# Kernel optimization log

Measured on AMD Instinct MI355X. Metric: run time of the kernel, lower is better.

## Reference

```python
import jax, jax.numpy as jnp
import numpy as np

H = 16
D_HEAD = 64  # model_dim // head_count = 1024 // 16
MODEL_DIM = 1024
MODEL_DIM1 = 768


def setup_inputs() -> dict:
    key = jax.random.key(0)
    ks = jax.random.split(key, 12)
    B, Q, K = 4, 1024, 1024
    inp = {
        "key": jax.random.normal(ks[0], (B, K, MODEL_DIM), jnp.float32),
        "value": jax.random.normal(ks[1], (B, K, MODEL_DIM), jnp.float32),
        "query": jax.random.normal(ks[2], (B, Q, MODEL_DIM1), jnp.float32),
        "mask": jax.random.randint(ks[3], (B, Q), 0, 2, jnp.int32),
        "additional_mask": jax.random.randint(ks[4], (B, K), 0, 2, jnp.int32),
        # learned params (nn.Linear weights stored as [in, out] for x @ W)
        "Wk": 0.02 * jax.random.normal(ks[5], (MODEL_DIM, H * D_HEAD), jnp.float32),
        "bk": jnp.zeros((H * D_HEAD,), jnp.float32),
        "Wv": 0.02 * jax.random.normal(ks[6], (MODEL_DIM, H * D_HEAD), jnp.float32),
        "bv": jnp.zeros((H * D_HEAD,), jnp.float32),
        "Wq": 0.02 * jax.random.normal(ks[7], (MODEL_DIM1, H * D_HEAD), jnp.float32),
        "bq": jnp.zeros((H * D_HEAD,), jnp.float32),
        "Wo": 0.02 * jax.random.normal(ks[8], (H * D_HEAD, MODEL_DIM1), jnp.float32),
        "bo": jnp.zeros((MODEL_DIM1,), jnp.float32),
    }
    return inp


def reference(key, value, query, mask, additional_mask, Wk, bk, Wv, bv, Wq, bq, Wo, bo):
    B, K_len = key.shape[0], key.shape[1]
    Q_len = query.shape[1]

    def shape(x):  # [B, L, H*d] -> [B, H, L, d]
        return x.reshape(B, -1, H, D_HEAD).transpose(0, 2, 1, 3)

    k = shape(key @ Wk + bk)
    v = shape(value @ Wv + bv)
    q = shape(query @ Wq + bq) / jnp.sqrt(jnp.float32(D_HEAD))

    scores = jnp.einsum("bhqd,bhkd->bhqk", q, k)  # [B,H,Q,K]
    top_score = scores[:, 0, :, :]  # pre-mask scores of head 0

    neg = jnp.float32(-1e18)
    scores = jnp.where(mask[:, None, :, None] == 0, neg, scores)
    scores = jnp.where(additional_mask[:, None, None, :] == 0, neg, scores)

    attn = jax.nn.softmax(scores, axis=-1)
    # dropout omitted (eval mode / deterministic reference)
    ctx = jnp.einsum("bhqk,bhkd->bhqd", attn, v)
    ctx = ctx.transpose(0, 2, 1, 3).reshape(B, Q_len, H * D_HEAD)
    output = ctx @ Wo + bo
    return output, top_score
```

## Files before the change

kernel.cpp:

```cpp
#include <hip/hip_runtime.h>
#include <hip/hip_bf16.h>

typedef __bf16 bf16_t;
typedef __bf16 bf16x8 __attribute__((ext_vector_type(8)));
typedef __bf16 bf16x4 __attribute__((ext_vector_type(4)));
typedef __bf16 bf16x2 __attribute__((ext_vector_type(2)));
typedef float  f32x4  __attribute__((ext_vector_type(4)));

#define MFMA16(a,b,c) __builtin_amdgcn_mfma_f32_16x16x32_bf16((a),(b),(c),0,0,0)

static constexpr int Bn = 4, Hn = 16, Dh = 64, SEQ = 1024;

template<int KD, int N, int MODE, typename AT>
__global__ __launch_bounds__(256)
void gemm_kernel(const AT* __restrict__ A, const float* __restrict__ W,
                 const float* __restrict__ bias, void* __restrict__ outp,
                 float scale)
{
    constexpr int BM = 128, BN = 64, BK = 32;
    __shared__ bf16_t As[BM][40];
    __shared__ bf16_t Bs[BN][40];
    const int t = threadIdx.x;
    const int lane = t & 63;
    const int w = t >> 6;
    const int wr = w >> 1, wc = w & 1;
    const int row0 = blockIdx.y * BM;
    const int col0 = blockIdx.x * BN;
    const int lrow = lane & 15;
    const int lk8  = (lane >> 4) * 8;

    const int ar = t >> 1, ac = (t & 1) * 16;
    const int bn0 = (t & 15) * 4, bk0 = (t >> 4) * 2;

    f32x4 acc[4][2] = {};

    f32x4  a_f[4];
    bf16x8 a_h[2];
    f32x4  b_r[2];

    auto loadA = [&](int kk) {
        if constexpr (sizeof(AT) == 4) {
            const float* src = (const float*)A + (size_t)(row0 + ar) * KD + kk + ac;
            a_f[0] = *(const f32x4*)(src + 0);
            a_f[1] = *(const f32x4*)(src + 4);
            a_f[2] = *(const f32x4*)(src + 8);
            a_f[3] = *(const f32x4*)(src + 12);
        } else {
            const bf16_t* src = (const bf16_t*)A + (size_t)(row0 + ar) * KD + kk + ac;
            a_h[0] = *(const bf16x8*)(src);
            a_h[1] = *(const bf16x8*)(src + 8);
        }
    };
    auto loadB = [&](int kk) {
        const float* src = W + (size_t)(kk + bk0) * N + col0 + bn0;
        b_r[0] = *(const f32x4*)(src);
        b_r[1] = *(const f32x4*)(src + N);
    };
    auto storeA = [&]() {
        bf16x8 v0, v1;
        if constexpr (sizeof(AT) == 4) {
            #pragma unroll
            for (int j = 0; j < 4; j++) {
                v0[j]     = (bf16_t)a_f[0][j];
                v0[4 + j] = (bf16_t)a_f[1][j];
                v1[j]     = (bf16_t)a_f[2][j];
                v1[4 + j] = (bf16_t)a_f[3][j];
            }
        } else { v0 = a_h[0]; v1 = a_h[1]; }
        *(bf16x8*)&As[ar][ac]     = v0;
        *(bf16x8*)&As[ar][ac + 8] = v1;
    };
    auto storeB = [&]() {
        #pragma unroll
        for (int c = 0; c < 4; c++) {
            bf16x2 p;
            p[0] = (bf16_t)b_r[0][c];
            p[1] = (bf16_t)b_r[1][c];
            *(bf16x2*)&Bs[bn0 + c][bk0] = p;
        }
    };

    loadA(0); loadB(0);
    for (int kk = 0; kk < KD; kk += BK) {
        storeA(); storeB();
        __syncthreads();
        if (kk + BK < KD) { loadA(kk + BK); loadB(kk + BK); }
        bf16x8 af[4], bfr[2];
        #pragma unroll
        for (int mf = 0; mf < 4; mf++)
            af[mf] = *(const bf16x8*)&As[wr * 64 + mf * 16 + lrow][lk8];
        #pragma unroll
        for (int nf = 0; nf < 2; nf++)
            bfr[nf] = *(const bf16x8*)&Bs[wc * 32 + nf * 16 + lrow][lk8];
        #pragma unroll
        for (int mf = 0; mf < 4; mf++)
            #pragma unroll
            for (int nf = 0; nf < 2; nf++)
                acc[mf][nf] = MFMA16(af[mf], bfr[nf], acc[mf][nf]);
        __syncthreads();
    }

    #pragma unroll
    for (int mf = 0; mf < 4; mf++) {
        #pragma unroll
        for (int nf = 0; nf < 2; nf++) {
            const int gcol = col0 + wc * 32 + nf * 16 + lrow;
            const float bv = bias[gcol];
            #pragma unroll
            for (int r = 0; r < 4; r++) {
                const int grow = row0 + wr * 64 + mf * 16 + (lane >> 4) * 4 + r;
                const float v = (acc[mf][nf][r] + bv) * scale;
                if constexpr (MODE == 0) {
                    const int b = grow >> 10, s = grow & 1023;
                    const int h = gcol >> 6, d = gcol & 63;
                    ((bf16_t*)outp)[((size_t)(b * Hn + h) * SEQ + s) * Dh + d] = (bf16_t)v;
                } else if constexpr (MODE == 1) {
                    const int b = grow >> 10, s = grow & 1023;
                    const int h = gcol >> 6, d = gcol & 63;
                    ((bf16_t*)outp)[((size_t)(b * Hn + h) * Dh + d) * SEQ + s] = (bf16_t)v;
                } else {
                    ((float*)outp)[(size_t)grow * N + gcol] = v;
                }
            }
        }
    }
}

__global__ __launch_bounds__(256)
void attn_kernel(const bf16_t* __restrict__ kbuf, const bf16_t* __restrict__ vT,
                 const bf16_t* __restrict__ qbuf, const int* __restrict__ qmask,
                 const int* __restrict__ kmask, bf16_t* __restrict__ ctx,
                 float* __restrict__ topsc)
{
    __shared__ bf16_t Pall[4][16 * 64];
    const int t = threadIdx.x, lane = t & 63, w = t >> 6;
    const int bidx = blockIdx.x;
    const int qt = bidx & 15, bh = bidx >> 4, b = bh >> 4, h = bh & 15;
    const int lrow = lane & 15, lk4 = lane >> 4, lk8 = lk4 * 8;
    const int wrow0 = qt * 64 + w * 16;
    const bf16_t* kb = kbuf + (size_t)bh * SEQ * Dh;
    const bf16_t* vb = vT + (size_t)bh * Dh * SEQ;
    char* Pw = (char*)&Pall[w][0];

    bf16x8 aq0, aq1;
    {
        const bf16_t* qp = qbuf + ((size_t)bh * SEQ + wrow0 + lrow) * Dh + lk8;
        aq0 = *(const bf16x8*)(qp);
        aq1 = *(const bf16x8*)(qp + 32);
    }
    int qmk[4];
    #pragma unroll
    for (int r = 0; r < 4; r++) qmk[r] = qmask[b * SEQ + wrow0 + lk4 * 4 + r];

    float m_run[4], l_run[4];
    #pragma unroll
    for (int r = 0; r < 4; r++) { m_run[r] = -__builtin_inff(); l_run[r] = 0.f; }
    f32x4 o[4] = {};

    bf16x8 kc0[4], kc1[4];
    #pragma unroll
    for (int nf = 0; nf < 4; nf++) {
        const bf16_t* kp = kb + (size_t)(nf * 16 + lrow) * Dh + lk8;
        kc0[nf] = *(const bf16x8*)(kp);
        kc1[nf] = *(const bf16x8*)(kp + 32);
    }

    for (int kt = 0; kt < 16; kt++) {
        const int key0 = kt * 64;
        bf16x8 vf0[4], vf1[4];
        #pragma unroll
        for (int nf = 0; nf < 4; nf++) {
            const bf16_t* vp = vb + (size_t)(nf * 16 + lrow) * SEQ + key0 + lk8;
            vf0[nf] = *(const bf16x8*)(vp);
            vf1[nf] = *(const bf16x8*)(vp + 32);
        }
        f32x4 s[4] = {};
        #pragma unroll
        for (int nf = 0; nf < 4; nf++) {
            s[nf] = MFMA16(aq0, kc0[nf], s[nf]);
            s[nf] = MFMA16(aq1, kc1[nf], s[nf]);
        }
        bf16x8 kn0[4], kn1[4];
        if (kt < 15) {
            #pragma unroll
            for (int nf = 0; nf < 4; nf++) {
                const bf16_t* kp = kb + (size_t)(key0 + 64 + nf * 16 + lrow) * Dh + lk8;
                kn0[nf] = *(const bf16x8*)(kp);
                kn1[nf] = *(const bf16x8*)(kp + 32);
            }
        }
        if (h == 0) {
            #pragma unroll
            for (int nf = 0; nf < 4; nf++)
                #pragma unroll
                for (int r = 0; r < 4; r++)
                    topsc[((size_t)b * SEQ + wrow0 + lk4 * 4 + r) * SEQ +
                          key0 + nf * 16 + lrow] = s[nf][r];
        }
        int km[4];
        #pragma unroll
        for (int nf = 0; nf < 4; nf++)
            km[nf] = kmask[b * SEQ + key0 + nf * 16 + lrow];
        float p[4][4], mt[4];
        #pragma unroll
        for (int r = 0; r < 4; r++) mt[r] = -__builtin_inff();
        #pragma unroll
        for (int nf = 0; nf < 4; nf++)
            #pragma unroll
            for (int r = 0; r < 4; r++) {
                const float sv = (qmk[r] && km[nf]) ? s[nf][r] : -1e18f;
                p[nf][r] = sv;
                mt[r] = fmaxf(mt[r], sv);
            }
        #pragma unroll
        for (int d = 1; d < 16; d <<= 1)
            #pragma unroll
            for (int r = 0; r < 4; r++) mt[r] = fmaxf(mt[r], __shfl_xor(mt[r], d));
        float resc[4], rs[4];
        #pragma unroll
        for (int r = 0; r < 4; r++) {
            const float mn = fmaxf(m_run[r], mt[r]);
            resc[r] = __expf(m_run[r] - mn);
            m_run[r] = mn;
            rs[r] = 0.f;
        }
        #pragma unroll
        for (int nf = 0; nf < 4; nf++)
            #pragma unroll
            for (int r = 0; r < 4; r++) {
                p[nf][r] = __expf(p[nf][r] - m_run[r]);
                rs[r] += p[nf][r];
            }
        #pragma unroll
        for (int d = 1; d < 16; d <<= 1)
            #pragma unroll
            for (int r = 0; r < 4; r++) rs[r] += __shfl_xor(rs[r], d);
        #pragma unroll
        for (int r = 0; r < 4; r++) l_run[r] = l_run[r] * resc[r] + rs[r];
        #pragma unroll
        for (int nf = 0; nf < 4; nf++)
            #pragma unroll
            for (int r = 0; r < 4; r++) o[nf][r] *= resc[r];
        #pragma unroll
        for (int nf = 0; nf < 4; nf++)
            #pragma unroll
            for (int r = 0; r < 4; r++) {
                const int prow = lk4 * 4 + r;
                const int pcol = nf * 16 + lrow;
                *(bf16_t*)(Pw + prow * 128 + ((pcol * 2) ^ ((prow & 7) << 4))) =
                    (bf16_t)p[nf][r];
            }
        bf16x8 pa[2];
        #pragma unroll
        for (int ks = 0; ks < 2; ks++) {
            const int coff = (ks * 32 + lk8) * 2;
            pa[ks] = *(const bf16x8*)(Pw + lrow * 128 + (coff ^ ((lrow & 7) << 4)));
        }
        #pragma unroll
        for (int nf = 0; nf < 4; nf++) {
            o[nf] = MFMA16(pa[0], vf0[nf], o[nf]);
            o[nf] = MFMA16(pa[1], vf1[nf], o[nf]);
        }
        #pragma unroll
        for (int nf = 0; nf < 4; nf++) { kc0[nf] = kn0[nf]; kc1[nf] = kn1[nf]; }
    }
    #pragma unroll
    for (int nf = 0; nf < 4; nf++)
        #pragma unroll
        for (int r = 0; r < 4; r++) {
            const int grow = wrow0 + lk4 * 4 + r;
            const float val = o[nf][r] / l_run[r];
            ctx[((size_t)b * SEQ + grow) * (Hn * Dh) + h * Dh + nf * 16 + lrow] =
                (bf16_t)val;
        }
}

extern "C" void kernel_launch(void* const* d_in, const int* in_sizes, int n_in,
                              void* d_out, int out_size, void* d_ws, size_t ws_size,
                              hipStream_t stream)
{
    const float* key   = (const float*)d_in[0];
    const float* value = (const float*)d_in[1];
    const float* query = (const float*)d_in[2];
    const int*   mask  = (const int*)d_in[3];
    const int*   amask = (const int*)d_in[4];
    const float* Wk = (const float*)d_in[5];
    const float* bk = (const float*)d_in[6];
    const float* Wv = (const float*)d_in[7];
    const float* bv = (const float*)d_in[8];
    const float* Wq = (const float*)d_in[9];
    const float* bq = (const float*)d_in[10];
    const float* Wo = (const float*)d_in[11];
    const float* bo = (const float*)d_in[12];

    const size_t per = (size_t)Bn * Hn * SEQ * Dh;
    bf16_t* kbuf = (bf16_t*)d_ws;
    bf16_t* vT   = kbuf + per;
    bf16_t* qbuf = vT + per;
    bf16_t* ctx  = qbuf + per;

    float* outf  = (float*)d_out;
    float* topsc = outf + (size_t)Bn * SEQ * 768;

    gemm_kernel<1024, 1024, 0, float><<<dim3(16, 32), 256, 0, stream>>>(key, Wk, bk, kbuf, 1.0f);
    gemm_kernel<1024, 1024, 1, float><<<dim3(16, 32), 256, 0, stream>>>(value, Wv, bv, vT, 1.0f);
    gemm_kernel<768, 1024, 0, float><<<dim3(16, 32), 256, 0, stream>>>(query, Wq, bq, qbuf, 0.125f);
    attn_kernel<<<dim3(Bn * Hn * 16), 256, 0, stream>>>(kbuf, vT, qbuf, mask, amask, ctx, topsc);
    gemm_kernel<1024, 768, 2, bf16_t><<<dim3(12, 32), 256, 0, stream>>>(ctx, Wo, bo, outf, 1.0f);
}
```

Measured before the change: 350.0 us.

## Pre-transpose weights to bf16, double-buffer GEMMs, split top-score kernel

Adds a kernel that converts and transposes all four weight matrices to bf16 once per call, so the GEMM can stage B tiles with direct global-to-LDS loads into double-buffered shared memory. GEMM outputs for the Q/K/V projections go through an LDS tile so the head-split and transposed layouts are written with coalesced vector stores. The attention kernel swaps the MFMA operand order so each lane owns one query row, which removes most shuffle reductions and vectorises the mask and P stores. The head-0 score writes move out of attention into a separate kernel that recomputes Q·K. The transposed weights are parked in the top_score region of the output buffer and overwritten by the final kernel; the extra launches and the recomputation add cost.

```diff
diff --git a/kernel.cpp b/kernel.cpp
--- a/kernel.cpp
+++ b/kernel.cpp
@@ -4,122 +4,181 @@
 typedef __bf16 bf16_t;
 typedef __bf16 bf16x8 __attribute__((ext_vector_type(8)));
 typedef __bf16 bf16x4 __attribute__((ext_vector_type(4)));
-typedef __bf16 bf16x2 __attribute__((ext_vector_type(2)));
 typedef float  f32x4  __attribute__((ext_vector_type(4)));
+typedef int    i32x4  __attribute__((ext_vector_type(4)));
 
 #define MFMA16(a,b,c) __builtin_amdgcn_mfma_f32_16x16x32_bf16((a),(b),(c),0,0,0)
 
 static constexpr int Bn = 4, Hn = 16, Dh = 64, SEQ = 1024;
+
+__device__ __forceinline__ void gll16(const void* g, void* l) {
+    __builtin_amdgcn_global_load_lds(
+        (const __attribute__((address_space(1))) void*)g,
+        (__attribute__((address_space(3))) void*)l, 16, 0, 0);
+}
+
+__global__ __launch_bounds__(256)
+void wtrans_kernel(const float* __restrict__ s0, const float* __restrict__ s1,
+                   const float* __restrict__ s2, const float* __restrict__ s3,
+                   bf16_t* __restrict__ d0, bf16_t* __restrict__ d1,
+                   bf16_t* __restrict__ d2, bf16_t* __restrict__ d3)
+{
+    __shared__ bf16_t tile[64][72];
+    const int bid = blockIdx.x, t = threadIdx.x;
+    const float* src; bf16_t* dst; int R, C, tr, tc;
+    if (bid < 256)      { src = s0; dst = d0; R = 1024; C = 1024; tr = bid >> 4;        tc = bid & 15; }
+    else if (bid < 512) { src = s1; dst = d1; R = 1024; C = 1024; tr = (bid-256) >> 4;  tc = (bid-256) & 15; }
+    else if (bid < 704) { src = s2; dst = d2; R = 768;  C = 1024; tr = (bid-512) >> 4;  tc = (bid-512) & 15; }
+    else                { src = s3; dst = d3; R = 1024; C = 768;  tr = (bid-704) / 12;  tc = (bid-704) % 12; }
+    const int r0 = tr * 64, c0 = tc * 64;
+    const int lr = t >> 2, lc0 = (t & 3) * 16;
+    #pragma unroll
+    for (int i = 0; i < 4; i++) {
+        f32x4 v = *(const f32x4*)&src[(size_t)(r0 + lr) * C + c0 + lc0 + i * 4];
+        #pragma unroll
+        for (int j = 0; j < 4; j++) tile[lr][lc0 + i * 4 + j] = (bf16_t)v[j];
+    }
+    __syncthreads();
+    const int oc = t >> 2, orc0 = (t & 3) * 16;
+    #pragma unroll
+    for (int i = 0; i < 2; i++) {
+        bf16x8 vv;
+        #pragma unroll
+        for (int j = 0; j < 8; j++) vv[j] = tile[orc0 + i * 8 + j][oc];
+        *(bf16x8*)&dst[(size_t)(c0 + oc) * R + r0 + orc0 + i * 8] = vv;
+    }
+}
 
 template<int KD, int N, int MODE, typename AT>
 __global__ __launch_bounds__(256)
-void gemm_kernel(const AT* __restrict__ A, const float* __restrict__ W,
-                 const float* __restrict__ bias, void* __restrict__ outp,
-                 float scale)
-{
-    constexpr int BM = 128, BN = 64, BK = 32;
-    __shared__ bf16_t As[BM][40];
-    __shared__ bf16_t Bs[BN][40];
-    const int t = threadIdx.x;
-    const int lane = t & 63;
-    const int w = t >> 6;
+void gemm_bt(const AT* __restrict__ A, const bf16_t* __restrict__ Bt,
+             const float* __restrict__ bias, void* __restrict__ outp,
+             float scale)
+{
+    __shared__ bf16_t As[2][128 * 32];
+    __shared__ bf16_t Bs[2][64 * 32];
+    __shared__ bf16_t Ct[(MODE == 2) ? 1 : 128 * 72];
+    const int t = threadIdx.x, lane = t & 63, w = t >> 6;
     const int wr = w >> 1, wc = w & 1;
-    const int row0 = blockIdx.y * BM;
-    const int col0 = blockIdx.x * BN;
-    const int lrow = lane & 15;
-    const int lk8  = (lane >> 4) * 8;
-
+    const int row0 = blockIdx.y * 128, col0 = blockIdx.x * 64;
+    const int lrow = lane & 15, lk4 = lane >> 4, lk8 = lk4 * 8;
     const int ar = t >> 1, ac = (t & 1) * 16;
-    const int bn0 = (t & 15) * 4, bk0 = (t >> 4) * 2;
 
     f32x4 acc[4][2] = {};
-
-    f32x4  a_f[4];
-    bf16x8 a_h[2];
-    f32x4  b_r[2];
-
-    auto loadA = [&](int kk) {
+    f32x4 a_f[4];
+
+    auto aload = [&](int kk) {
         if constexpr (sizeof(AT) == 4) {
             const float* src = (const float*)A + (size_t)(row0 + ar) * KD + kk + ac;
-            a_f[0] = *(const f32x4*)(src + 0);
+            a_f[0] = *(const f32x4*)(src);
             a_f[1] = *(const f32x4*)(src + 4);
             a_f[2] = *(const f32x4*)(src + 8);
             a_f[3] = *(const f32x4*)(src + 12);
-        } else {
-            const bf16_t* src = (const bf16_t*)A + (size_t)(row0 + ar) * KD + kk + ac;
-            a_h[0] = *(const bf16x8*)(src);
-            a_h[1] = *(const bf16x8*)(src + 8);
         }
     };
-    auto loadB = [&](int kk) {
-        const float* src = W + (size_t)(kk + bk0) * N + col0 + bn0;
-        b_r[0] = *(const f32x4*)(src);
-        b_r[1] = *(const f32x4*)(src + N);
+    auto awrite = [&](int buf) {
+        if constexpr (sizeof(AT) == 4) {
+            bf16x8 v0, v1;
+            #pragma unroll
+            for (int j = 0; j < 4; j++) {
+                v0[j] = (bf16_t)a_f[0][j]; v0[4 + j] = (bf16_t)a_f[1][j];
+                v1[j] = (bf16_t)a_f[2][j]; v1[4 + j] = (bf16_t)a_f[3][j];
+            }
+            *(bf16x8*)&As[buf][ar * 32 + ac]     = v0;
+            *(bf16x8*)&As[buf][ar * 32 + ac + 8] = v1;
+        }
     };
-    auto storeA = [&]() {
-        bf16x8 v0, v1;
-        if constexpr (sizeof(AT) == 4) {
-            #pragma unroll
-            for (int j = 0; j < 4; j++) {
-                v0[j]     = (bf16_t)a_f[0][j];
-                v0[4 + j] = (bf16_t)a_f[1][j];
-                v1[j]     = (bf16_t)a_f[2][j];
-                v1[4 + j] = (bf16_t)a_f[3][j];
-            }
-        } else { v0 = a_h[0]; v1 = a_h[1]; }
-        *(bf16x8*)&As[ar][ac]     = v0;
-        *(bf16x8*)&As[ar][ac + 8] = v1;
+    auto astage_gll = [&](int buf, int kk) {
+        if constexpr (sizeof(AT) == 2) {
+            #pragma unroll
+            for (int j = 0; j < 2; j++) {
+                const int idx = j * 256 + t;
+                const bf16_t* g = (const bf16_t*)A +
+                    (size_t)(row0 + (idx >> 2)) * KD + kk + (idx & 3) * 8;
+                gll16(g, &As[buf][(j * 256 + w * 64) * 8]);
+            }
+        }
     };
-    auto storeB = [&]() {
-        #pragma unroll
-        for (int c = 0; c < 4; c++) {
-            bf16x2 p;
-            p[0] = (bf16_t)b_r[0][c];
-            p[1] = (bf16_t)b_r[1][c];
-            *(bf16x2*)&Bs[bn0 + c][bk0] = p;
-        }
+    auto bstage = [&](int buf, int kk) {
+        const bf16_t* g = Bt + (size_t)(col0 + (t >> 2)) * KD + kk + (t & 3) * 8;
+        gll16(g, &Bs[buf][w * 512]);
     };
 
-    loadA(0); loadB(0);
-    for (int kk = 0; kk < KD; kk += BK) {
-        storeA(); storeB();
+    constexpr int NB = KD / 32;
+    if constexpr (sizeof(AT) == 4) { aload(0); awrite(0); }
+    else                            astage_gll(0, 0);
+    bstage(0, 0);
+
+    for (int s = 0; s < NB; s++) {
         __syncthreads();
-        if (kk + BK < KD) { loadA(kk + BK); loadB(kk + BK); }
+        const int cur = s & 1;
+        if (s + 1 < NB) {
+            bstage(cur ^ 1, (s + 1) * 32);
+            if constexpr (sizeof(AT) == 4) aload((s + 1) * 32);
+            else                           astage_gll(cur ^ 1, (s + 1) * 32);
+        }
         bf16x8 af[4], bfr[2];
         #pragma unroll
         for (int mf = 0; mf < 4; mf++)
-            af[mf] = *(const bf16x8*)&As[wr * 64 + mf * 16 + lrow][lk8];
+            af[mf] = *(const bf16x8*)&As[cur][(wr * 64 + mf * 16 + lrow) * 32 + lk8];
         #pragma unroll
         for (int nf = 0; nf < 2; nf++)
-            bfr[nf] = *(const bf16x8*)&Bs[wc * 32 + nf * 16 + lrow][lk8];
+            bfr[nf] = *(const bf16x8*)&Bs[cur][(wc * 32 + nf * 16 + lrow) * 32 + lk8];
         #pragma unroll
         for (int mf = 0; mf < 4; mf++)
             #pragma unroll
             for (int nf = 0; nf < 2; nf++)
                 acc[mf][nf] = MFMA16(af[mf], bfr[nf], acc[mf][nf]);
+        if (s + 1 < NB) { if constexpr (sizeof(AT) == 4) awrite(cur ^ 1); }
+    }
+
+    if constexpr (MODE == 2) {
+        #pragma unroll
+        for (int mf = 0; mf < 4; mf++)
+            #pragma unroll
+            for (int nf = 0; nf < 2; nf++) {
+                const int gcol = col0 + wc * 32 + nf * 16 + lrow;
+                const float bv = bias[gcol];
+                #pragma unroll
+                for (int r = 0; r < 4; r++) {
+                    const int grow = row0 + wr * 64 + mf * 16 + lk4 * 4 + r;
+                    ((float*)outp)[(size_t)grow * N + gcol] = (acc[mf][nf][r] + bv) * scale;
+                }
+            }
+    } else {
         __syncthreads();
-    }
-
-    #pragma unroll
-    for (int mf = 0; mf < 4; mf++) {
-        #pragma unroll
-        for (int nf = 0; nf < 2; nf++) {
-            const int gcol = col0 + wc * 32 + nf * 16 + lrow;
-            const float bv = bias[gcol];
-            #pragma unroll
-            for (int r = 0; r < 4; r++) {
-                const int grow = row0 + wr * 64 + mf * 16 + (lane >> 4) * 4 + r;
-                const float v = (acc[mf][nf][r] + bv) * scale;
-                if constexpr (MODE == 0) {
-                    const int b = grow >> 10, s = grow & 1023;
-                    const int h = gcol >> 6, d = gcol & 63;
-                    ((bf16_t*)outp)[((size_t)(b * Hn + h) * SEQ + s) * Dh + d] = (bf16_t)v;
-                } else if constexpr (MODE == 1) {
-                    const int b = grow >> 10, s = grow & 1023;
-                    const int h = gcol >> 6, d = gcol & 63;
-                    ((bf16_t*)outp)[((size_t)(b * Hn + h) * Dh + d) * SEQ + s] = (bf16_t)v;
-                } else {
-                    ((float*)outp)[(size_t)grow * N + gcol] = v;
+        #pragma unroll
+        for (int mf = 0; mf < 4; mf++)
+            #pragma unroll
+            for (int nf = 0; nf < 2; nf++) {
+                const int lcol = wc * 32 + nf * 16 + lrow;
+                const float bv = bias[col0 + lcol];
+                #pragma unroll
+                for (int r = 0; r < 4; r++)
+                    Ct[(wr * 64 + mf * 16 + lk4 * 4 + r) * 72 + lcol] =
+                        (bf16_t)((acc[mf][nf][r] + bv) * scale);
+            }
+        __syncthreads();
+        const int h = col0 >> 6, b = row0 >> 10;
+        bf16_t* op = (bf16_t*)outp + ((size_t)(b * Hn + h) << 16);
+        if constexpr (MODE == 0) {
+            #pragma unroll
+            for (int j = 0; j < 4; j++) {
+                const int sl = j * 32 + (t >> 3), cl0 = (t & 7) * 8;
+                bf16x8 v = *(const bf16x8*)&Ct[sl * 72 + cl0];
+                *(bf16x8*)&op[(size_t)((row0 & 1023) + sl) * 64 + cl0] = v;
+            }
+        } else {
+            #pragma unroll
+            for (int jj = 0; jj < 2; jj++) {
+                const int cl = jj * 32 + (t >> 3);
+                #pragma unroll
+                for (int k = 0; k < 2; k++) {
+                    const int sl0 = k * 64 + (t & 7) * 8;
+                    bf16x8 v;
+                    #pragma unroll
+                    for (int i = 0; i < 8; i++) v[i] = Ct[(sl0 + i) * 72 + cl];
+                    *(bf16x8*)&op[(size_t)cl * 1024 + (row0 & 1023) + sl0] = v;
                 }
             }
         }
@@ -129,8 +188,7 @@
 __global__ __launch_bounds__(256)
 void attn_kernel(const bf16_t* __restrict__ kbuf, const bf16_t* __restrict__ vT,
                  const bf16_t* __restrict__ qbuf, const int* __restrict__ qmask,
-                 const int* __restrict__ kmask, bf16_t* __restrict__ ctx,
-                 float* __restrict__ topsc)
+                 const int* __restrict__ kmask, bf16_t* __restrict__ ctx)
 {
     __shared__ bf16_t Pall[4][16 * 64];
     const int t = threadIdx.x, lane = t & 63, w = t >> 6;
@@ -141,6 +199,7 @@
     const bf16_t* kb = kbuf + (size_t)bh * SEQ * Dh;
     const bf16_t* vb = vT + (size_t)bh * Dh * SEQ;
     char* Pw = (char*)&Pall[w][0];
+    const int sw = (lrow & 7) << 4;
 
     bf16x8 aq0, aq1;
     {
@@ -148,13 +207,9 @@
         aq0 = *(const bf16x8*)(qp);
         aq1 = *(const bf16x8*)(qp + 32);
     }
-    int qmk[4];
-    #pragma unroll
-    for (int r = 0; r < 4; r++) qmk[r] = qmask[b * SEQ + wrow0 + lk4 * 4 + r];
-
-    float m_run[4], l_run[4];
-    #pragma unroll
-    for (int r = 0; r < 4; r++) { m_run[r] = -__builtin_inff(); l_run[r] = 0.f; }
+    const int qm = qmask[b * SEQ + wrow0 + lrow];
+
+    float m_run = -__builtin_inff(), l_run = 0.f;
     f32x4 o[4] = {};
 
     bf16x8 kc0[4], kc1[4];
@@ -174,11 +229,15 @@
             vf0[nf] = *(const bf16x8*)(vp);
             vf1[nf] = *(const bf16x8*)(vp + 32);
         }
-        f32x4 s[4] = {};
-        #pragma unroll
-        for (int nf = 0; nf < 4; nf++) {
-            s[nf] = MFMA16(aq0, kc0[nf], s[nf]);
-            s[nf] = MFMA16(aq1, kc1[nf], s[nf]);
+        i32x4 km[4];
+        #pragma unroll
+        for (int nf = 0; nf < 4; nf++)
+            km[nf] = *(const i32x4*)&kmask[b * SEQ + key0 + nf * 16 + lk4 * 4];
+        f32x4 s4[4] = {};
+        #pragma unroll
+        for (int nf = 0; nf < 4; nf++) {
+            s4[nf] = MFMA16(kc0[nf], aq0, s4[nf]);
+            s4[nf] = MFMA16(kc1[nf], aq1, s4[nf]);
         }
         bf16x8 kn0[4], kn1[4];
         if (kt < 15) {
@@ -189,90 +248,99 @@
                 kn1[nf] = *(const bf16x8*)(kp + 32);
             }
         }
-        if (h == 0) {
-            #pragma unroll
-            for (int nf = 0; nf < 4; nf++)
-                #pragma unroll
-                for (int r = 0; r < 4; r++)
-                    topsc[((size_t)b * SEQ + wrow0 + lk4 * 4 + r) * SEQ +
-                          key0 + nf * 16 + lrow] = s[nf][r];
-        }
-        int km[4];
-        #pragma unroll
-        for (int nf = 0; nf < 4; nf++)
-            km[nf] = kmask[b * SEQ + key0 + nf * 16 + lrow];
-        float p[4][4], mt[4];
-        #pragma unroll
-        for (int r = 0; r < 4; r++) mt[r] = -__builtin_inff();
+        float p[4][4];
+        float mt = m_run;
         #pragma unroll
         for (int nf = 0; nf < 4; nf++)
             #pragma unroll
             for (int r = 0; r < 4; r++) {
-                const float sv = (qmk[r] && km[nf]) ? s[nf][r] : -1e18f;
+                const float sv = (qm && km[nf][r]) ? s4[nf][r] : -1e18f;
                 p[nf][r] = sv;
-                mt[r] = fmaxf(mt[r], sv);
-            }
-        #pragma unroll
-        for (int d = 1; d < 16; d <<= 1)
-            #pragma unroll
-            for (int r = 0; r < 4; r++) mt[r] = fmaxf(mt[r], __shfl_xor(mt[r], d));
-        float resc[4], rs[4];
-        #pragma unroll
-        for (int r = 0; r < 4; r++) {
-            const float mn = fmaxf(m_run[r], mt[r]);
-            resc[r] = __expf(m_run[r] - mn);
-            m_run[r] = mn;
-            rs[r] = 0.f;
-        }
+                mt = fmaxf(mt, sv);
+            }
+        mt = fmaxf(mt, __shfl_xor(mt, 16));
+        mt = fmaxf(mt, __shfl_xor(mt, 32));
+        const float resc = __expf(m_run - mt);
+        m_run = mt;
+        float rs = 0.f;
         #pragma unroll
         for (int nf = 0; nf < 4; nf++)
             #pragma unroll
             for (int r = 0; r < 4; r++) {
-                p[nf][r] = __expf(p[nf][r] - m_run[r]);
-                rs[r] += p[nf][r];
-            }
-        #pragma unroll
-        for (int d = 1; d < 16; d <<= 1)
-            #pragma unroll
-            for (int r = 0; r < 4; r++) rs[r] += __shfl_xor(rs[r], d);
-        #pragma unroll
-        for (int r = 0; r < 4; r++) l_run[r] = l_run[r] * resc[r] + rs[r];
-        #pragma unroll
-        for (int nf = 0; nf < 4; nf++)
-            #pragma unroll
-            for (int r = 0; r < 4; r++) o[nf][r] *= resc[r];
-        #pragma unroll
-        for (int nf = 0; nf < 4; nf++)
-            #pragma unroll
-            for (int r = 0; r < 4; r++) {
-                const int prow = lk4 * 4 + r;
-                const int pcol = nf * 16 + lrow;
-                *(bf16_t*)(Pw + prow * 128 + ((pcol * 2) ^ ((prow & 7) << 4))) =
-                    (bf16_t)p[nf][r];
-            }
-        bf16x8 pa[2];
-        #pragma unroll
-        for (int ks = 0; ks < 2; ks++) {
-            const int coff = (ks * 32 + lk8) * 2;
-            pa[ks] = *(const bf16x8*)(Pw + lrow * 128 + (coff ^ ((lrow & 7) << 4)));
-        }
-        #pragma unroll
-        for (int nf = 0; nf < 4; nf++) {
-            o[nf] = MFMA16(pa[0], vf0[nf], o[nf]);
-            o[nf] = MFMA16(pa[1], vf1[nf], o[nf]);
+                p[nf][r] = __expf(p[nf][r] - m_run);
+                rs += p[nf][r];
+            }
+        rs += __shfl_xor(rs, 16);
+        rs += __shfl_xor(rs, 32);
+        l_run = l_run * resc + rs;
+        #pragma unroll
+        for (int nf = 0; nf < 4; nf++)
+            #pragma unroll
+            for (int r = 0; r < 4; r++) o[nf][r] *= resc;
+        #pragma unroll
+        for (int nf = 0; nf < 4; nf++) {
+            bf16x4 pk;
+            #pragma unroll
+            for (int r = 0; r < 4; r++) pk[r] = (bf16_t)p[nf][r];
+            *(bf16x4*)(Pw + lrow * 128 + ((nf * 32 + lk4 * 8) ^ sw)) = pk;
+        }
+        bf16x8 pa0 = *(const bf16x8*)(Pw + lrow * 128 + ((lk4 * 16) ^ sw));
+        bf16x8 pa1 = *(const bf16x8*)(Pw + lrow * 128 + ((64 + lk4 * 16) ^ sw));
+        #pragma unroll
+        for (int nf = 0; nf < 4; nf++) {
+            o[nf] = MFMA16(vf0[nf], pa0, o[nf]);
+            o[nf] = MFMA16(vf1[nf], pa1, o[nf]);
         }
         #pragma unroll
         for (int nf = 0; nf < 4; nf++) { kc0[nf] = kn0[nf]; kc1[nf] = kn1[nf]; }
     }
+    const float inv = 1.0f / l_run;
     #pragma unroll
-    for (int nf = 0; nf < 4; nf++)
-        #pragma unroll
-        for (int r = 0; r < 4; r++) {
-            const int grow = wrow0 + lk4 * 4 + r;
-            const float val = o[nf][r] / l_run[r];
-            ctx[((size_t)b * SEQ + grow) * (Hn * Dh) + h * Dh + nf * 16 + lrow] =
-                (bf16_t)val;
-        }
+    for (int nf = 0; nf < 4; nf++) {
+        bf16x4 pk;
+        #pragma unroll
+        for (int r = 0; r < 4; r++) pk[r] = (bf16_t)(o[nf][r] * inv);
+        *(bf16x4*)(Pw + lrow * 128 + ((nf * 32 + lk4 * 8) ^ sw)) = pk;
+    }
+    const int qp2 = lane >> 2, ch = lane & 3;
+    const int sw2 = (qp2 & 7) << 4;
+    bf16x8 o0 = *(const bf16x8*)(Pw + qp2 * 128 + ((ch * 32) ^ sw2));
+    bf16x8 o1 = *(const bf16x8*)(Pw + qp2 * 128 + ((ch * 32 + 16) ^ sw2));
+    bf16_t* cp = ctx + ((size_t)(b * SEQ + wrow0 + qp2)) * 1024 + h * 64 + ch * 16;
+    *(bf16x8*)cp = o0;
+    *(bf16x8*)(cp + 8) = o1;
+}
+
+__global__ __launch_bounds__(256)
+void topsc_kernel(const bf16_t* __restrict__ kbuf, const bf16_t* __restrict__ qbuf,
+                  float* __restrict__ topsc)
+{
+    const int t = threadIdx.x, lane = t & 63, w = t >> 6;
+    const int bx = blockIdx.x;
+    const int b = bx >> 6, qt = (bx >> 2) & 15, kq = bx & 3;
+    const int lrow = lane & 15, lk4 = lane >> 4, lk8 = lk4 * 8;
+    const int wrow0 = qt * 64 + w * 16;
+    const bf16_t* kb = kbuf + ((size_t)(b * Hn)) * SEQ * Dh;
+    const bf16_t* qp = qbuf + ((size_t)(b * Hn)) * SEQ * Dh
+                     + (size_t)(wrow0 + lrow) * Dh + lk8;
+    bf16x8 aq0 = *(const bf16x8*)(qp);
+    bf16x8 aq1 = *(const bf16x8*)(qp + 32);
+    for (int kt = 0; kt < 4; kt++) {
+        const int key0 = kq * 256 + kt * 64;
+        f32x4 s4[4] = {};
+        #pragma unroll
+        for (int nf = 0; nf < 4; nf++) {
+            const bf16_t* kp = kb + (size_t)(key0 + nf * 16 + lrow) * Dh + lk8;
+            s4[nf] = MFMA16(aq0, *(const bf16x8*)(kp), s4[nf]);
+            s4[nf] = MFMA16(aq1, *(const bf16x8*)(kp + 32), s4[nf]);
+        }
+        #pragma unroll
+        for (int nf = 0; nf < 4; nf++)
+            #pragma unroll
+            for (int r = 0; r < 4; r++)
+                topsc[(size_t)(b * SEQ + wrow0 + lk4 * 4 + r) * SEQ +
+                      key0 + nf * 16 + lrow] = s4[nf][r];
+    }
 }
 
 extern "C" void kernel_launch(void* const* d_in, const int* in_sizes, int n_in,
@@ -294,17 +362,23 @@
     const float* bo = (const float*)d_in[12];
 
     const size_t per = (size_t)Bn * Hn * SEQ * Dh;
-    bf16_t* kbuf = (bf16_t*)d_ws;
-    bf16_t* vT   = kbuf + per;
-    bf16_t* qbuf = vT + per;
-    bf16_t* ctx  = qbuf + per;
-
-    float* outf  = (float*)d_out;
+    bf16_t* kproj = (bf16_t*)d_ws;
+    bf16_t* vT    = kproj + per;
+    bf16_t* qproj = vT + per;
+    bf16_t* ctx   = qproj + per;
+
+    float* outf = (float*)d_out;
+    bf16_t* WkT = (bf16_t*)(outf + (size_t)Bn * SEQ * 768);
+    bf16_t* WvT = WkT + 1024 * 1024;
+    bf16_t* WqT = WvT + 1024 * 1024;
+    bf16_t* WoT = WqT + 1024 * 768;
     float* topsc = outf + (size_t)Bn * SEQ * 768;
 
-    gemm_kernel<1024, 1024, 0, float><<<dim3(16, 32), 256, 0, stream>>>(key, Wk, bk, kbuf, 1.0f);
-    gemm_kernel<1024, 1024, 1, float><<<dim3(16, 32), 256, 0, stream>>>(value, Wv, bv, vT, 1.0f);
-    gemm_kernel<768, 1024, 0, float><<<dim3(16, 32), 256, 0, stream>>>(query, Wq, bq, qbuf, 0.125f);
-    attn_kernel<<<dim3(Bn * Hn * 16), 256, 0, stream>>>(kbuf, vT, qbuf, mask, amask, ctx, topsc);
-    gemm_kernel<1024, 768, 2, bf16_t><<<dim3(12, 32), 256, 0, stream>>>(ctx, Wo, bo, outf, 1.0f);
-}
+    wtrans_kernel<<<896, 256, 0, stream>>>(Wk, Wv, Wq, Wo, WkT, WvT, WqT, WoT);
+    gemm_bt<1024, 1024, 0, float><<<dim3(16, 32), 256, 0, stream>>>(key,   WkT, bk, kproj, 1.0f);
+    gemm_bt<1024, 1024, 1, float><<<dim3(16, 32), 256, 0, stream>>>(value, WvT, bv, vT,    1.0f);
+    gemm_bt< 768, 1024, 0, float><<<dim3(16, 32), 256, 0, stream>>>(query, WqT, bq, qproj, 0.125f);
+    attn_kernel<<<dim3(Bn * Hn * 16), 256, 0, stream>>>(kproj, vT, qproj, mask, amask, ctx);
+    gemm_bt<1024, 768, 2, bf16_t><<<dim3(12, 32), 256, 0, stream>>>(ctx, WoT, bo, outf, 1.0f);
+    topsc_kernel<<<256, 256, 0, stream>>>(kproj, qproj, topsc);
+}
```

Measured after the change: 369.2 us. +5.5%, slower.
